# Optimization experiments

Measured on AMD Instinct MI355X. Metric: run time of the kernel, lower is better.

## Reference

```python
import jax, jax.numpy as jnp
import numpy as np

N, CIN, T = 10000, 64, 64
COUT, K = 64, 3


def setup_inputs() -> dict:
    key = jax.random.key(0)
    k1, k2, k3 = jax.random.split(key, 3)
    x = jax.random.normal(k1, (N, CIN, T), dtype=jnp.float32)
    # torch Conv1d default init: uniform(-1/sqrt(fan_in), 1/sqrt(fan_in))
    bound = 1.0 / np.sqrt(CIN * K)
    weight = jax.random.uniform(k2, (2 * COUT, CIN, K), dtype=jnp.float32, minval=-bound, maxval=bound)
    bias = jax.random.uniform(k3, (2 * COUT,), dtype=jnp.float32, minval=-bound, maxval=bound)
    return {"x": x, "weight": weight, "bias": bias}


def reference(x, weight, bias):
    # Batched 1D conv over time for all nodes at once (equivalent to the
    # per-node loop in the original, since weights are shared).
    # x: [N, Cin, T], weight: [2*Cout, Cin, K] -> y: [N, 2*Cout, T-K+1]
    y = jax.lax.conv_general_dilated(
        x, weight, window_strides=(1,), padding="VALID",
        dimension_numbers=("NCH", "OIH", "NCH"))
    y = y + bias[None, :, None]
    # GLU along channel dim: first half gated by sigmoid of second half
    a, b = jnp.split(y, 2, axis=1)
    return a * jax.nn.sigmoid(b)
```

## Files before the change

### kernel.cpp

```cpp
#include <hip/hip_runtime.h>
#include <hip/hip_bf16.h>

typedef __attribute__((ext_vector_type(8))) short short8;
typedef __attribute__((ext_vector_type(4))) float float4v;
typedef __attribute__((ext_vector_type(2))) unsigned int uint2v;
typedef __attribute__((ext_vector_type(4))) unsigned int uint4v;

#define NSAMP 10000
#define CIN   64
#define TLEN  64
#define COUT  64
#define TOUT  62

static __device__ __forceinline__ ushort f2bf(float v) {
    unsigned int x = __float_as_uint(v);
    return (ushort)((x + 0x7fffu + ((x >> 16) & 1u)) >> 16);
}

static __device__ __forceinline__ unsigned int cvt_pk_bf16(float a, float b) {
    unsigned int r;
    asm("v_cvt_pk_bf16_f32 %0, %1, %2" : "=v"(r) : "v"(a), "v"(b));
    return r;
}

__global__ void prep_weights(const float* __restrict__ w, ushort* __restrict__ wa) {
    int o = blockIdx.x * blockDim.x + threadIdx.x;
    if (o >= 128 * 192) return;
    int co = o / 192;
    int kk = o - co * 192;
    int k  = kk >> 6;
    int ci = kk & 63;
    wa[o] = f2bf(w[co * 192 + ci * 3 + k]);
}

__global__ __launch_bounds__(256, 8)
void prep_x(const float* __restrict__ x, ushort* __restrict__ xt) {
    __shared__ __align__(16) ushort b[64 * 64];
    const int n   = blockIdx.x;
    const int tid = threadIdx.x;

    const int cig = tid >> 4;
    const int ts  = (tid & 15) * 4;
    const float* p = x + (long)n * (CIN * TLEN) + cig * 4 * TLEN + ts;
    float4v v0 = *(const float4v*)(p);
    float4v v1 = *(const float4v*)(p + TLEN);
    float4v v2 = *(const float4v*)(p + 2 * TLEN);
    float4v v3 = *(const float4v*)(p + 3 * TLEN);
    char* base = (char*)b;
#pragma unroll
    for (int r = 0; r < 4; ++r) {
        int t = ts + r;
        uint2v val;
        val.x = cvt_pk_bf16(v0[r], v1[r]);
        val.y = cvt_pk_bf16(v2[r], v3[r]);
        *(uint2v*)(base + t * 128 + ((cig * 8) ^ ((t & 7) << 4))) = val;
    }
    __syncthreads();

    char* outn = (char*)(xt + (long)n * (TLEN * CIN));
#pragma unroll
    for (int i = 0; i < 2; ++i) {
        int f = i * 256 + tid;
        int t = f >> 3, c = f & 7;
        uint4v val = *(const uint4v*)(base + t * 128 + ((c * 16) ^ ((t & 7) << 4)));
        *(uint4v*)(outn + f * 16) = val;
    }
}

__global__ __launch_bounds__(512, 4)
void conv_glu_xt(const ushort* __restrict__ xt, const ushort* __restrict__ wa,
                 const float* __restrict__ bias, float* __restrict__ out) {
    const int tid = threadIdx.x;
    const int w   = tid >> 6;
    const int L   = tid & 63;
    const int l   = L & 15;
    const int q   = L >> 4;
    const int h2  = w & 3;
    const int nh  = w >> 2;
    const int t0  = nh * 32;

    short8 afr[2][6];
#pragma unroll
    for (int mt = 0; mt < 2; ++mt) {
        int co = 64 * mt + 16 * h2 + l;
        const short8* wrow = (const short8*)(wa + co * 192);
#pragma unroll
        for (int kc = 0; kc < 6; ++kc)
            afr[mt][kc] = wrow[kc * 4 + q];
    }

    float bv[4], bg[4];
#pragma unroll
    for (int r = 0; r < 4; ++r) {
        bv[r] = bias[16 * h2 + 4 * q + r];
        bg[r] = bias[64 + 16 * h2 + 4 * q + r];
    }

    const int stride = gridDim.x;
    for (int n = blockIdx.x; n < NSAMP; n += stride) {
        const char* bbase = (const char*)(xt + (long)n * (TLEN * CIN))
                            + (t0 + l) * 128 + q * 16;

        float4v acc[2][2];
#pragma unroll
        for (int nt = 0; nt < 2; ++nt) {
            acc[0][nt] = (float4v){bv[0], bv[1], bv[2], bv[3]};
            acc[1][nt] = (float4v){bg[0], bg[1], bg[2], bg[3]};
        }

#pragma unroll
        for (int kc = 0; kc < 6; ++kc) {
            const int tap = kc >> 1;
            const int cib = (kc & 1) * 64;
#pragma unroll
            for (int nt = 0; nt < 2; ++nt) {
                const short8 bfr = *(const short8*)(bbase + (nt * 16 + tap) * 128 + cib);
                acc[0][nt] = __builtin_amdgcn_mfma_f32_16x16x32_bf16(
                    afr[0][kc], bfr, acc[0][nt], 0, 0, 0);
                acc[1][nt] = __builtin_amdgcn_mfma_f32_16x16x32_bf16(
                    afr[1][kc], bfr, acc[1][nt], 0, 0, 0);
            }
        }

        char* obase = (char*)out + (long)n * (COUT * TOUT * 4)
                      + (16 * h2 + 4 * q) * (TOUT * 4) + (t0 + l) * 4;
#pragma unroll
        for (int nt = 0; nt < 2; ++nt) {
            int t = t0 + nt * 16 + l;
            if (t < TOUT) {
#pragma unroll
                for (int r = 0; r < 4; ++r) {
                    float g  = acc[1][nt][r];
                    float sg = 1.0f / (1.0f + __expf(-g));
                    *(float*)(obase + r * (TOUT * 4) + nt * 64) = acc[0][nt][r] * sg;
                }
            }
        }
    }
}

__global__ __launch_bounds__(256, 4)
void conv_glu(const float* __restrict__ x, const ushort* __restrict__ wa,
              const float* __restrict__ bias, float* __restrict__ out) {
    __shared__ __align__(16) ushort xT[64 * 64];

    const int n   = blockIdx.x;
    const int tid = threadIdx.x;
    const int w   = tid >> 6;
    const int L   = tid & 63;
    const int l   = L & 15;
    const int q   = L >> 4;
    const int h   = w & 1;
    const int nh  = w >> 1;
    const int t0base = nh * 32;

    const float* xs = x + n * (CIN * TLEN);
    {
        const int cig = tid >> 4;
        const int ts  = (tid & 15) * 4;
        const float* p = xs + cig * 4 * TLEN + ts;
        float4v v0 = *(const float4v*)(p);
        float4v v1 = *(const float4v*)(p + TLEN);
        float4v v2 = *(const float4v*)(p + 2 * TLEN);
        float4v v3 = *(const float4v*)(p + 3 * TLEN);
        char* base = (char*)xT;
#pragma unroll
        for (int r = 0; r < 4; ++r) {
            int t = ts + r;
            uint2v val;
            val.x = cvt_pk_bf16(v0[r], v1[r]);
            val.y = cvt_pk_bf16(v2[r], v3[r]);
            *(uint2v*)(base + t * 128 + ((cig * 8) ^ ((t & 7) << 4))) = val;
        }
    }
    __syncthreads();

    const ushort* arow[4];
#pragma unroll
    for (int mt = 0; mt < 4; ++mt) {
        int co = 32 * h + 16 * (mt & 1) + 64 * (mt >> 1) + l;
        arow[mt] = wa + co * 192 + q * 8;
    }

    float4v acc[4][2];
#pragma unroll
    for (int mt = 0; mt < 4; ++mt)
#pragma unroll
        for (int nt = 0; nt < 2; ++nt)
            acc[mt][nt] = (float4v){0.f, 0.f, 0.f, 0.f};

#pragma unroll
    for (int kc = 0; kc < 6; ++kc) {
        short8 afr[4];
#pragma unroll
        for (int mt = 0; mt < 4; ++mt)
            afr[mt] = *(const short8*)(arow[mt] + kc * 32);

        const int tap  = kc >> 1;
        const int cib2 = (kc & 1) * 64 + q * 16;
#pragma unroll
        for (int nt = 0; nt < 2; ++nt) {
            int t = t0base + nt * 16 + l + tap;
            if (t > 63) t = 63;
            const short8 bfr = *(const short8*)((const char*)xT + t * 128
                                                + (cib2 ^ ((t & 7) << 4)));
#pragma unroll
            for (int mt = 0; mt < 4; ++mt)
                acc[mt][nt] = __builtin_amdgcn_mfma_f32_16x16x32_bf16(
                    afr[mt], bfr, acc[mt][nt], 0, 0, 0);
        }
    }

#pragma unroll
    for (int p2 = 0; p2 < 2; ++p2)
#pragma unroll
        for (int nt = 0; nt < 2; ++nt)
#pragma unroll
            for (int r = 0; r < 4; ++r) {
                int co = 32 * h + 16 * p2 + 4 * q + r;
                int t  = t0base + nt * 16 + l;
                float a = acc[p2][nt][r]     + bias[co];
                float g = acc[p2 + 2][nt][r] + bias[co + 64];
                float sg = 1.0f / (1.0f + __expf(-g));
                if (t < TOUT)
                    out[(n * COUT + co) * TOUT + t] = a * sg;
            }
}

extern "C" void kernel_launch(void* const* d_in, const int* in_sizes, int n_in,
                              void* d_out, int out_size, void* d_ws, size_t ws_size,
                              hipStream_t stream) {
    const float* x    = (const float*)d_in[0];
    const float* wt   = (const float*)d_in[1];
    const float* bias = (const float*)d_in[2];
    ushort*      wa   = (ushort*)d_ws;
    float*       out  = (float*)d_out;

    prep_weights<<<96, 256, 0, stream>>>(wt, wa);

    const size_t need = 65536 + (size_t)NSAMP * TLEN * CIN * 2 + 4096;
    if (ws_size >= need) {
        ushort* xxt = (ushort*)((char*)d_ws + 65536);
        prep_x<<<NSAMP, 256, 0, stream>>>(x, xxt);
        conv_glu_xt<<<2048, 512, 0, stream>>>(xxt, wa, bias, out);
    } else {
        conv_glu<<<NSAMP, 256, 0, stream>>>(x, wa, bias, out);
    }
}
```

Before: 408.5 us.

## Stage transposed samples into LDS with async triple-buffered loads in conv kernel

The conv kernel now gives each block a fixed run of 8 samples. Each sample's bf16 tile is streamed into a 3-deep LDS ring using global_load_lds, with hand-placed vmcnt waits and barriers so the next tiles load while the current one runs its MFMAs. The B fragments are read from swizzled LDS instead of straight from global memory. prep_x handles two samples per block and writes in a swizzled layout. This adds manual waitcnt bookkeeping that must match the number of outstanding loads, including the output stores, and any mismatch would be a correctness risk.

```diff
diff --git a/kernel.cpp b/kernel.cpp
--- a/kernel.cpp
+++ b/kernel.cpp
@@ -11,6 +11,9 @@
 #define TLEN  64
 #define COUT  64
 #define TOUT  62
+#define SPX   2
+#define SPW   8
+#define CONVBLK (NSAMP / SPW)
 
 static __device__ __forceinline__ ushort f2bf(float v) {
     unsigned int x = __float_as_uint(v);
@@ -21,6 +24,12 @@
     unsigned int r;
     asm("v_cvt_pk_bf16_f32 %0, %1, %2" : "=v"(r) : "v"(a), "v"(b));
     return r;
+}
+
+static __device__ __forceinline__ void stage16(const void* g, void* l) {
+    typedef __attribute__((address_space(1))) const unsigned int guint;
+    typedef __attribute__((address_space(3))) unsigned int luint;
+    __builtin_amdgcn_global_load_lds((guint*)g, (luint*)l, 16, 0, 0);
 }
 
 __global__ void prep_weights(const float* __restrict__ w, ushort* __restrict__ wa) {
@@ -36,48 +45,56 @@
 __global__ __launch_bounds__(256, 8)
 void prep_x(const float* __restrict__ x, ushort* __restrict__ xt) {
     __shared__ __align__(16) ushort b[64 * 64];
-    const int n   = blockIdx.x;
     const int tid = threadIdx.x;
-
-    const int cig = tid >> 4;
-    const int ts  = (tid & 15) * 4;
-    const float* p = x + (long)n * (CIN * TLEN) + cig * 4 * TLEN + ts;
-    float4v v0 = *(const float4v*)(p);
-    float4v v1 = *(const float4v*)(p + TLEN);
-    float4v v2 = *(const float4v*)(p + 2 * TLEN);
-    float4v v3 = *(const float4v*)(p + 3 * TLEN);
-    char* base = (char*)b;
-#pragma unroll
-    for (int r = 0; r < 4; ++r) {
-        int t = ts + r;
-        uint2v val;
-        val.x = cvt_pk_bf16(v0[r], v1[r]);
-        val.y = cvt_pk_bf16(v2[r], v3[r]);
-        *(uint2v*)(base + t * 128 + ((cig * 8) ^ ((t & 7) << 4))) = val;
-    }
-    __syncthreads();
-
-    char* outn = (char*)(xt + (long)n * (TLEN * CIN));
-#pragma unroll
-    for (int i = 0; i < 2; ++i) {
-        int f = i * 256 + tid;
-        int t = f >> 3, c = f & 7;
-        uint4v val = *(const uint4v*)(base + t * 128 + ((c * 16) ^ ((t & 7) << 4)));
-        *(uint4v*)(outn + f * 16) = val;
+    const int w   = tid >> 6;
+    const int L   = tid & 63;
+    const int a   = L & 31;
+    const int g   = L >> 5;
+    const int tb  = 16 * w + 8 * g;
+    const long n0 = (long)blockIdx.x * SPX;
+    char* lb = (char*)b;
+
+    const float* p0 = x + n0 * (CIN * TLEN) + (2 * a) * TLEN + tb;
+    float4v A0 = *(const float4v*)(p0);
+    float4v A1 = *(const float4v*)(p0 + 4);
+    float4v A2 = *(const float4v*)(p0 + TLEN);
+    float4v A3 = *(const float4v*)(p0 + TLEN + 4);
+    const float* p1 = p0 + CIN * TLEN;
+    float4v B0 = *(const float4v*)(p1);
+    float4v B1 = *(const float4v*)(p1 + 4);
+    float4v B2 = *(const float4v*)(p1 + TLEN);
+    float4v B3 = *(const float4v*)(p1 + TLEN + 4);
+
+#pragma unroll
+    for (int s = 0; s < SPX; ++s) {
+        float4v lo0 = s ? B0 : A0, lo1 = s ? B1 : A1;
+        float4v hi0 = s ? B2 : A2, hi1 = s ? B3 : A3;
+#pragma unroll
+        for (int j = 0; j < 8; ++j) {
+            int t = tb + j;
+            float xa  = (j < 4) ? lo0[j & 3] : lo1[j & 3];
+            float xb_ = (j < 4) ? hi0[j & 3] : hi1[j & 3];
+            unsigned int val = cvt_pk_bf16(xa, xb_);
+            *(unsigned int*)(lb + t * 128 + ((4 * a) ^ ((t & 7) << 4))) = val;
+        }
+        char* dst = (char*)xt + (n0 + s) * (TLEN * CIN * 2);
+        int o1 = w * 2048 + L * 16;
+        uint4v d1 = *(const uint4v*)(lb + o1);
+        uint4v d2 = *(const uint4v*)(lb + o1 + 1024);
+        *(uint4v*)(dst + o1) = d1;
+        *(uint4v*)(dst + o1 + 1024) = d2;
     }
 }
 
 __global__ __launch_bounds__(512, 4)
 void conv_glu_xt(const ushort* __restrict__ xt, const ushort* __restrict__ wa,
                  const float* __restrict__ bias, float* __restrict__ out) {
+    __shared__ __align__(16) ushort xb[3][66 * 64];
+
     const int tid = threadIdx.x;
-    const int w   = tid >> 6;
-    const int L   = tid & 63;
-    const int l   = L & 15;
-    const int q   = L >> 4;
-    const int h2  = w & 3;
-    const int nh  = w >> 2;
-    const int t0  = nh * 32;
+    const int w  = tid >> 6, L = tid & 63, l = L & 15, q = L >> 4;
+    const int h2 = w & 3, nh = w >> 2, t0 = nh * 32;
+    const long n0 = (long)blockIdx.x * SPW;
 
     short8 afr[2][6];
 #pragma unroll
@@ -88,7 +105,6 @@
         for (int kc = 0; kc < 6; ++kc)
             afr[mt][kc] = wrow[kc * 4 + q];
     }
-
     float bv[4], bg[4];
 #pragma unroll
     for (int r = 0; r < 4; ++r) {
@@ -96,11 +112,18 @@
         bg[r] = bias[64 + 16 * h2 + 4 * q + r];
     }
 
-    const int stride = gridDim.x;
-    for (int n = blockIdx.x; n < NSAMP; n += stride) {
-        const char* bbase = (const char*)(xt + (long)n * (TLEN * CIN))
-                            + (t0 + l) * 128 + q * 16;
-
+    const char* gs = (const char*)xt + n0 * 8192 + tid * 16;
+    stage16(gs + 0 * 8192, &xb[0][tid * 8]);
+    stage16(gs + 1 * 8192, &xb[1][tid * 8]);
+    asm volatile("s_waitcnt vmcnt(1)" ::: "memory");
+    asm volatile("s_barrier" ::: "memory");
+
+#pragma unroll
+    for (int s = 0; s < SPW; ++s) {
+        if (s + 2 < SPW)
+            stage16(gs + (long)(s + 2) * 8192, &xb[(s + 2) % 3][tid * 8]);
+
+        const char* rb = (const char*)&xb[s % 3][0];
         float4v acc[2][2];
 #pragma unroll
         for (int nt = 0; nt < 2; ++nt) {
@@ -111,10 +134,12 @@
 #pragma unroll
         for (int kc = 0; kc < 6; ++kc) {
             const int tap = kc >> 1;
-            const int cib = (kc & 1) * 64;
+            const int cib = (kc & 1) * 64 + q * 16;
 #pragma unroll
             for (int nt = 0; nt < 2; ++nt) {
-                const short8 bfr = *(const short8*)(bbase + (nt * 16 + tap) * 128 + cib);
+                int t = t0 + nt * 16 + l + tap;
+                const short8 bfr = *(const short8*)(rb + t * 128
+                                                    + (cib ^ ((t & 7) << 4)));
                 acc[0][nt] = __builtin_amdgcn_mfma_f32_16x16x32_bf16(
                     afr[0][kc], bfr, acc[0][nt], 0, 0, 0);
                 acc[1][nt] = __builtin_amdgcn_mfma_f32_16x16x32_bf16(
@@ -122,17 +147,24 @@
             }
         }
 
-        char* obase = (char*)out + (long)n * (COUT * TOUT * 4)
-                      + (16 * h2 + 4 * q) * (TOUT * 4) + (t0 + l) * 4;
+        if (s + 1 < SPW) {
+            if (s == 0)      asm volatile("s_waitcnt vmcnt(1)" ::: "memory");
+            else if (s < 6)  asm volatile("s_waitcnt vmcnt(9)" ::: "memory");
+            else             asm volatile("s_waitcnt vmcnt(8)" ::: "memory");
+            asm volatile("s_barrier" ::: "memory");
+        }
+
+        char* ob = (char*)out + (n0 + s) * (COUT * TOUT * 4)
+                   + (16 * h2 + 4 * q) * (TOUT * 4) + (t0 + l) * 4;
 #pragma unroll
         for (int nt = 0; nt < 2; ++nt) {
             int t = t0 + nt * 16 + l;
             if (t < TOUT) {
 #pragma unroll
                 for (int r = 0; r < 4; ++r) {
-                    float g  = acc[1][nt][r];
-                    float sg = 1.0f / (1.0f + __expf(-g));
-                    *(float*)(obase + r * (TOUT * 4) + nt * 64) = acc[0][nt][r] * sg;
+                    float g2 = acc[1][nt][r];
+                    float sg = 1.0f / (1.0f + __expf(-g2));
+                    *(float*)(ob + r * (TOUT * 4) + nt * 64) = acc[0][nt][r] * sg;
                 }
             }
         }
@@ -241,8 +273,8 @@
     const size_t need = 65536 + (size_t)NSAMP * TLEN * CIN * 2 + 4096;
     if (ws_size >= need) {
         ushort* xxt = (ushort*)((char*)d_ws + 65536);
-        prep_x<<<NSAMP, 256, 0, stream>>>(x, xxt);
-        conv_glu_xt<<<2048, 512, 0, stream>>>(xxt, wa, bias, out);
+        prep_x<<<NSAMP / SPX, 256, 0, stream>>>(x, xxt);
+        conv_glu_xt<<<CONVBLK, 512, 0, stream>>>(xxt, wa, bias, out);
     } else {
         conv_glu<<<NSAMP, 256, 0, stream>>>(x, wa, bias, out);
     }
```

New measurement: 327.7 us. -19.8%, faster.
